# Kernel optimization log

Hardware: AMD Instinct MI355X
Metric: run time of the kernel (lower is better)

Reference implementation:

```python
import jax, jax.numpy as jnp
import numpy as np

NUM_INPUTS = 6
NUM_MFS = 3
BATCH = 32768


def _rule_table():
    # torch.cartesian_prod over NUM_INPUTS copies of arange(NUM_MFS)
    grids = np.meshgrid(*[np.arange(NUM_MFS)] * NUM_INPUTS, indexing='ij')
    return np.stack(grids, axis=-1).reshape(-1, NUM_INPUTS)  # [R, I], R = M**I


def setup_inputs() -> dict:
    key = jax.random.key(0)
    k1, k2, k3, k4 = jax.random.split(key, 4)
    num_rules = NUM_MFS ** NUM_INPUTS
    x = jax.random.normal(k1, (BATCH, NUM_INPUTS), dtype=jnp.float32)
    # params initialized like torch.rand -> uniform(0,1); sigmas stay positive
    centers = jax.random.uniform(k2, (NUM_INPUTS, NUM_MFS), dtype=jnp.float32)
    sigmas = jax.random.uniform(k3, (NUM_INPUTS, NUM_MFS), dtype=jnp.float32)
    rule_weights = jax.random.uniform(k4, (num_rules, NUM_INPUTS + 1), dtype=jnp.float32)
    return {"x": x, "centers": centers, "sigmas": sigmas, "rule_weights": rule_weights}


def reference(x, centers, sigmas, rule_weights):
    B, I = x.shape
    M = centers.shape[1]
    rules = jnp.asarray(_rule_table())  # [R, I] int, constant
    # Gaussian membership: [B, I, M]
    mf = jnp.exp(-0.5 * ((x[:, :, None] - centers) / sigmas) ** 2)
    mf = mf.transpose(0, 2, 1)  # [B, M, I] (matches permute(0,2,1))
    # strengths[b, r] = prod_i mf[b, rules[r, i], i]
    gathered = mf[:, rules, jnp.arange(I)]  # [B, R, I]
    strengths = jnp.prod(gathered, axis=-1)  # [B, R]
    norm = strengths / jnp.sum(strengths, axis=1, keepdims=True)
    xb = jnp.concatenate([x, jnp.ones((B, 1), dtype=x.dtype)], axis=1)  # [B, I+1]
    rule_out = xb @ rule_weights.T  # [B, R]
    out = jnp.sum(norm * rule_out, axis=1, keepdims=True)  # [B, 1]
    return jax.nn.sigmoid(out)
```

## Files before the change

kernel.cpp:

```cpp
#include <hip/hip_runtime.h>

#define NI 6
#define NM 3
#define NR 729
#define PART_RULES 243
#define BLK_ELEMS 64
#define NPART 3
#define NTHREADS (BLK_ELEMS * NPART)
#define BATCH 32768

__global__ __launch_bounds__(NTHREADS) void anfis_kernel(
    const float* __restrict__ x,
    const float* __restrict__ centers,
    const float* __restrict__ sigmas,
    const float* __restrict__ rw,
    float* __restrict__ out)
{
    __shared__ float wlds[NR * 8];
    __shared__ float red_num[NPART - 1][BLK_ELEMS];
    __shared__ float red_den[NPART - 1][BLK_ELEMS];

    const int lx   = threadIdx.x;
    const int part = threadIdx.y;
    const int tid  = lx + BLK_ELEMS * part;

    for (int r = tid; r < NR; r += NTHREADS) {
        const float* src = rw + r * 7;
        float* dst = wlds + r * 8;
        #pragma unroll
        for (int j = 0; j < 7; ++j) dst[j] = src[j];
        dst[7] = 0.0f;
    }

    const int elem = blockIdx.x * BLK_ELEMS + lx;
    const float* xp = x + elem * NI;
    float xv[NI];
    #pragma unroll
    for (int i = 0; i < NI; ++i) xv[i] = xp[i];

    float mf[NI][NM];
    #pragma unroll
    for (int i = 0; i < NI; ++i) {
        float z[NM];
        #pragma unroll
        for (int m = 0; m < NM; ++m) {
            const float t = (xv[i] - centers[i * NM + m]) *
                            __builtin_amdgcn_rcpf(sigmas[i * NM + m]);
            z[m] = t * t;
        }
        const float zmin = fminf(fminf(z[0], z[1]), z[2]);
        #pragma unroll
        for (int m = 0; m < NM; ++m)
            mf[i][m] = __expf(-0.5f * (z[m] - zmin));
    }

    __syncthreads();

    float g45[9];
    #pragma unroll
    for (int m4 = 0; m4 < 3; ++m4)
        #pragma unroll
        for (int m5 = 0; m5 < 3; ++m5)
            g45[m4 * 3 + m5] = mf[4][m4] * mf[5][m5];

    const float a0 = mf[0][part];
    float num = 0.0f, den = 0.0f;
    int r = part * PART_RULES;
    for (int m1 = 0; m1 < 3; ++m1) {
        const float a1 = a0 * mf[1][m1];
        for (int m2 = 0; m2 < 3; ++m2) {
            const float a2 = a1 * mf[2][m2];
            #pragma unroll
            for (int m3 = 0; m3 < 3; ++m3) {
                const float a3 = a2 * mf[3][m3];
                #pragma unroll
                for (int k = 0; k < 9; ++k) {
                    const float s = a3 * g45[k];
                    const float4 wa = *reinterpret_cast<const float4*>(&wlds[(r + k) * 8]);
                    const float4 wb = *reinterpret_cast<const float4*>(&wlds[(r + k) * 8 + 4]);
                    float ro = wb.z;
                    ro = fmaf(xv[0], wa.x, ro);
                    ro = fmaf(xv[1], wa.y, ro);
                    ro = fmaf(xv[2], wa.z, ro);
                    ro = fmaf(xv[3], wa.w, ro);
                    ro = fmaf(xv[4], wb.x, ro);
                    ro = fmaf(xv[5], wb.y, ro);
                    num = fmaf(s, ro, num);
                    den += s;
                }
                r += 9;
            }
        }
    }

    if (part != 0) {
        red_num[part - 1][lx] = num;
        red_den[part - 1][lx] = den;
    }
    __syncthreads();
    if (part == 0) {
        num += red_num[0][lx] + red_num[1][lx];
        den += red_den[0][lx] + red_den[1][lx];
        const float t = num * __builtin_amdgcn_rcpf(den);
        const float e = __expf(-t);
        out[elem] = __builtin_amdgcn_rcpf(1.0f + e);
    }
}

extern "C" void kernel_launch(void* const* d_in, const int* in_sizes, int n_in,
                              void* d_out, int out_size, void* d_ws, size_t ws_size,
                              hipStream_t stream) {
    const float* x       = (const float*)d_in[0];
    const float* centers = (const float*)d_in[1];
    const float* sigmas  = (const float*)d_in[2];
    const float* rw      = (const float*)d_in[3];
    float* out           = (float*)d_out;

    dim3 block(BLK_ELEMS, NPART, 1);
    dim3 grid(BATCH / BLK_ELEMS, 1, 1);
    hipLaunchKernelGGL(anfis_kernel, grid, block, 0, stream,
                       x, centers, sigmas, rw, out);
}
```

Before: 73.42 us.

## Split rules across nine parts and compute denominator as product of MF sums

Raises the number of rule partitions per element from three to nine, fixing the first two membership indices per thread slice and fully unrolling the remaining 81-rule loop. The per-rule denominator accumulation is dropped and replaced by the factorised product of per-input membership sums, computed once at the end. Three independent numerator accumulators shorten the FMA dependency chain. The block grows to 576 threads, which adds more reduction traffic through shared memory and may lower occupancy through register or thread limits.

```diff
diff --git a/kernel.cpp b/kernel.cpp
--- a/kernel.cpp
+++ b/kernel.cpp
@@ -3,9 +3,9 @@
 #define NI 6
 #define NM 3
 #define NR 729
-#define PART_RULES 243
+#define NPART 9
+#define PART_RULES 81
 #define BLK_ELEMS 64
-#define NPART 3
 #define NTHREADS (BLK_ELEMS * NPART)
 #define BATCH 32768
 
@@ -18,11 +18,12 @@
 {
     __shared__ float wlds[NR * 8];
     __shared__ float red_num[NPART - 1][BLK_ELEMS];
-    __shared__ float red_den[NPART - 1][BLK_ELEMS];
 
     const int lx   = threadIdx.x;
     const int part = threadIdx.y;
     const int tid  = lx + BLK_ELEMS * part;
+    const int m0   = part / 3;
+    const int m1   = part % 3;
 
     for (int r = tid; r < NR; r += NTHREADS) {
         const float* src = rw + r * 7;
@@ -63,45 +64,47 @@
         for (int m5 = 0; m5 < 3; ++m5)
             g45[m4 * 3 + m5] = mf[4][m4] * mf[5][m5];
 
-    const float a0 = mf[0][part];
-    float num = 0.0f, den = 0.0f;
+    const float a01 = mf[0][m0] * mf[1][m1];
+    float num0 = 0.0f, num1 = 0.0f, num2 = 0.0f;
     int r = part * PART_RULES;
-    for (int m1 = 0; m1 < 3; ++m1) {
-        const float a1 = a0 * mf[1][m1];
-        for (int m2 = 0; m2 < 3; ++m2) {
-            const float a2 = a1 * mf[2][m2];
+    #pragma unroll
+    for (int m2 = 0; m2 < 3; ++m2) {
+        const float a2 = a01 * mf[2][m2];
+        #pragma unroll
+        for (int m3 = 0; m3 < 3; ++m3) {
+            const float a3 = a2 * mf[3][m3];
             #pragma unroll
-            for (int m3 = 0; m3 < 3; ++m3) {
-                const float a3 = a2 * mf[3][m3];
-                #pragma unroll
-                for (int k = 0; k < 9; ++k) {
-                    const float s = a3 * g45[k];
-                    const float4 wa = *reinterpret_cast<const float4*>(&wlds[(r + k) * 8]);
-                    const float4 wb = *reinterpret_cast<const float4*>(&wlds[(r + k) * 8 + 4]);
-                    float ro = wb.z;
-                    ro = fmaf(xv[0], wa.x, ro);
-                    ro = fmaf(xv[1], wa.y, ro);
-                    ro = fmaf(xv[2], wa.z, ro);
-                    ro = fmaf(xv[3], wa.w, ro);
-                    ro = fmaf(xv[4], wb.x, ro);
-                    ro = fmaf(xv[5], wb.y, ro);
-                    num = fmaf(s, ro, num);
-                    den += s;
-                }
-                r += 9;
+            for (int k = 0; k < 9; ++k) {
+                const float s = a3 * g45[k];
+                const float4 wa = *reinterpret_cast<const float4*>(&wlds[(r + k) * 8]);
+                const float4 wb = *reinterpret_cast<const float4*>(&wlds[(r + k) * 8 + 4]);
+                float ro = wb.z;
+                ro = fmaf(xv[0], wa.x, ro);
+                ro = fmaf(xv[1], wa.y, ro);
+                ro = fmaf(xv[2], wa.z, ro);
+                ro = fmaf(xv[3], wa.w, ro);
+                ro = fmaf(xv[4], wb.x, ro);
+                ro = fmaf(xv[5], wb.y, ro);
+                if (k % 3 == 0)      num0 = fmaf(s, ro, num0);
+                else if (k % 3 == 1) num1 = fmaf(s, ro, num1);
+                else                 num2 = fmaf(s, ro, num2);
             }
+            r += 9;
         }
     }
+    const float num = (num0 + num1) + num2;
 
-    if (part != 0) {
-        red_num[part - 1][lx] = num;
-        red_den[part - 1][lx] = den;
-    }
+    if (part != 0) red_num[part - 1][lx] = num;
     __syncthreads();
     if (part == 0) {
-        num += red_num[0][lx] + red_num[1][lx];
-        den += red_den[0][lx] + red_den[1][lx];
-        const float t = num * __builtin_amdgcn_rcpf(den);
+        float ntot = num;
+        #pragma unroll
+        for (int j = 0; j < NPART - 1; ++j) ntot += red_num[j][lx];
+        float den = 1.0f;
+        #pragma unroll
+        for (int i = 0; i < NI; ++i)
+            den *= (mf[i][0] + mf[i][1]) + mf[i][2];
+        const float t = ntot * __builtin_amdgcn_rcpf(den);
         const float e = __expf(-t);
         out[elem] = __builtin_amdgcn_rcpf(1.0f + e);
     }
```

Result: faster. 71.23 us (-3.0%).
